# Performance work log

Hardware: AMD Instinct MI355X
Metric: run time of the kernel (lower is better)

The kernel has to match this reference:

```python
import jax, jax.numpy as jnp
import numpy as np

N_NODES, IN_DIM, HID, LAT, N_EDGES = 50000, 3000, 512, 30, 800000
NEG_SLOPE = 0.2


def setup_inputs() -> dict:
    key = jax.random.key(0)
    ks = jax.random.split(key, 6)
    x = jax.random.normal(ks[0], (N_NODES, IN_DIM), dtype=jnp.float32)
    edge_index = jax.random.randint(ks[1], (2, N_EDGES), 0, N_NODES, dtype=jnp.int64)
    # xavier-normal-ish scales
    W1 = jax.random.normal(ks[2], (IN_DIM, HID), dtype=jnp.float32) * 0.02
    W2 = jax.random.normal(ks[3], (HID, LAT), dtype=jnp.float32) * 0.06
    att_src = jax.random.normal(ks[4], (HID,), dtype=jnp.float32) * 0.1
    att_dst = jax.random.normal(ks[5], (HID,), dtype=jnp.float32) * 0.1
    return {"x": x, "edge_index": edge_index, "W1": W1, "W2": W2,
            "att_src": att_src, "att_dst": att_dst}


def _segment_softmax(e, seg, num_segments):
    # numerically stable softmax over variable-degree dst neighborhoods
    m = jax.ops.segment_max(e, seg, num_segments=num_segments)
    m = jnp.where(jnp.isfinite(m), m, 0.0)  # empty segments -> 0, harmless
    p = jnp.exp(e - m[seg])
    s = jax.ops.segment_sum(p, seg, num_segments=num_segments)
    return p / (s[seg] + 1e-16)


def reference(x, edge_index, W1, W2, att_src, att_dst):
    N = x.shape[0]
    src, dst = edge_index[0], edge_index[1]  # messages flow src(j) -> dst(i)

    # ---- conv1: full GAT layer (heads=1, no self-loops, no bias) ----
    h1 = x @ W1                                   # [N, 512]
    a_src = h1 @ att_src                          # [N]
    a_dst = h1 @ att_dst                          # [N]
    e = jax.nn.leaky_relu(a_src[src] + a_dst[dst], NEG_SLOPE)  # [E]
    alpha = _segment_softmax(e, dst, N)           # [E] (also tied attn for conv3)
    agg1 = jax.ops.segment_sum(h1[src] * alpha[:, None], dst, num_segments=N)
    x1 = jax.nn.elu(agg1)                         # [N, 512]

    # ---- conv2: attention=False -> plain linear projection ----
    x2 = x1 @ W2                                  # [N, 30] (latent embedding)

    # ---- conv3: tied weights (W2^T) + tied attention from conv1 ----
    h3 = x2 @ W2.T                                # [N, 512]
    agg3 = jax.ops.segment_sum(h3[src] * alpha[:, None], dst, num_segments=N)
    x3 = jax.nn.elu(agg3)

    # ---- conv4: attention=False, tied weights (W1^T) ----
    x4 = x3 @ W1.T                                # [N, in_channels]
    return (x2, x4)
```

## Files before the change

kernel.cpp:

```cpp
#include <hip/hip_runtime.h>

#define N_NODES 50000
#define IN_DIM  3000
#define HID     512
#define LAT     30
#define N_EDGES 800000
#define M_PAD   50048
#define K1_PAD  3008
#define N4_PAD  3072

typedef __bf16 bf16;
typedef unsigned int uint;
typedef __attribute__((ext_vector_type(4))) float f32x4;
typedef __attribute__((ext_vector_type(8))) bf16 bf16x8;

__device__ __forceinline__ float bf2f(bf16 b){ return (float)b; }

__device__ __forceinline__ void gl16(const void* g, void* l){
  __builtin_amdgcn_global_load_lds(
      (const __attribute__((address_space(1))) void*)g,
      (__attribute__((address_space(3))) void*)l, 16, 0, 0);
}

__device__ __forceinline__ int xcd_swz(int orig, int nwg){
  int q = nwg >> 3, r = nwg & 7;
  int xcd = orig & 7, lid = orig >> 3;
  return (xcd < r ? xcd*(q+1) : r*(q+1) + (xcd-r)*q) + lid;
}

__device__ __forceinline__ bf16x8 cvt8v(f32x4 a, f32x4 b){
  bf16x8 r;
  r[0]=(bf16)a[0]; r[1]=(bf16)a[1]; r[2]=(bf16)a[2]; r[3]=(bf16)a[3];
  r[4]=(bf16)b[0]; r[5]=(bf16)b[1]; r[6]=(bf16)b[2]; r[7]=(bf16)b[3];
  return r;
}

__global__ void k_w1t(const float* __restrict__ W1, bf16* __restrict__ W1T){
  int k = blockIdx.x*256 + threadIdx.x;
  int n = blockIdx.y;
  if (k >= K1_PAD) return;
  float v = (k < IN_DIM) ? W1[(long)k*HID + n] : 0.f;
  W1T[(long)n*K1_PAD + k] = (bf16)v;
}
__global__ void k_w1p(const float* __restrict__ W1, bf16* __restrict__ W1P){
  int k = blockIdx.x*256 + threadIdx.x;
  int n = blockIdx.y;
  if (k >= HID) return;
  float v = (n < IN_DIM) ? W1[(long)n*HID + k] : 0.f;
  W1P[(long)n*HID + k] = (bf16)v;
}
__global__ void k_w2t(const float* __restrict__ W2, bf16* __restrict__ W2T){
  int k = blockIdx.x*256 + threadIdx.x;
  int n = blockIdx.y;
  if (k >= HID) return;
  float v = (n < LAT) ? W2[(long)k*LAT + n] : 0.f;
  W2T[(long)n*HID + k] = (bf16)v;
}
__global__ void k_w2p(const float* __restrict__ W2, bf16* __restrict__ W2P){
  int t = blockIdx.x*256 + threadIdx.x;
  if (t >= HID*32) return;
  int n = t >> 5, k = t & 31;
  W2P[t] = (bf16)((k < LAT) ? W2[(long)n*LAT + k] : 0.f);
}

__global__ __launch_bounds__(256) void gemm_xw1(
    const float* __restrict__ X, const bf16* __restrict__ Bw, bf16* __restrict__ C)
{
  __shared__ float Af[2][128*32];
  __shared__ bf16  Bl[2][128*32];
  const int NBX = HID/128;
  const int tid  = threadIdx.x;
  const int lane = tid & 63;
  const int w    = tid >> 6;
  const int wm   = (w >> 1) * 64, wn = (w & 1) * 64;
  const int wgid = xcd_swz(blockIdx.x, gridDim.x);
  const int col0 = (wgid % NBX) * 128, row0 = (wgid / NBX) * 128;

  f32x4 acc[4][4];
  #pragma unroll
  for (int mi=0;mi<4;mi++)
    #pragma unroll
    for (int ni=0;ni<4;ni++)
      acc[mi][ni] = (f32x4){0.f,0.f,0.f,0.f};

  const int ar  = tid >> 3;
  const int apc = tid & 7;
  const int ac4 = (apc ^ (ar & 7)) * 4;
  int aoff[4];
  #pragma unroll
  for (int i=0;i<4;i++)
    aoff[i] = min(row0 + i*32 + ar, N_NODES-1) * IN_DIM;

  const int sr = tid >> 2;
  const int sc = (tid & 3) * 16;
  const char* gB = (const char*)(Bw + (long)(col0 + sr) * K1_PAD) + sc;
  const long bstep = (long)64 * K1_PAD * 2;

#define STAGE1(buf, ks) do{                                             \
    int kcl_ = min((ks)*32 + ac4, IN_DIM-4);                            \
    char* lA_ = (char*)&Af[buf][0] + tid*16;                            \
    _Pragma("unroll")                                                   \
    for (int i_=0;i_<4;i_++)                                            \
      gl16(X + aoff[i_] + kcl_, lA_ + i_*4096);                         \
    char* lB_ = (char*)&Bl[buf][0] + sr*64 + sc;                        \
    gl16(gB + (long)(ks)*64,         lB_);                              \
    gl16(gB + (long)(ks)*64 + bstep, lB_ + 64*64);                      \
  }while(0)

  STAGE1(0, 0);
  asm volatile("s_waitcnt vmcnt(0)" ::: "memory");
  __builtin_amdgcn_s_barrier();

  for (int ks = 0; ks < 94; ks++){
    const int cur = ks & 1;
    if (ks + 1 < 94) STAGE1(cur^1, ks+1);

    const float* Ac = &Af[cur][0];
    const bf16*  Bc = &Bl[cur][0];
    const int g2 = (lane >> 4) * 2;
    bf16x8 af[4], bfr[4];
    #pragma unroll
    for (int mi=0;mi<4;mi++){
      int row = wm + mi*16 + (lane & 15);
      int rx  = row & 7;
      f32x4 f0 = *(const f32x4*)&Ac[row*32 + ((g2    ) ^ rx)*4];
      f32x4 f1 = *(const f32x4*)&Ac[row*32 + ((g2 + 1) ^ rx)*4];
      af[mi] = cvt8v(f0, f1);
    }
    #pragma unroll
    for (int ni=0;ni<4;ni++)
      bfr[ni] = *(const bf16x8*)&Bc[(wn + ni*16 + (lane & 15))*32 + (lane>>4)*8];
    #pragma unroll
    for (int mi=0;mi<4;mi++)
      #pragma unroll
      for (int ni=0;ni<4;ni++)
        acc[mi][ni] = __builtin_amdgcn_mfma_f32_16x16x32_bf16(af[mi], bfr[ni], acc[mi][ni], 0, 0, 0);

    asm volatile("s_waitcnt vmcnt(0)" ::: "memory");
    __builtin_amdgcn_s_barrier();
  }
#undef STAGE1

  const int crb  = (lane >> 4) * 4;
  const int ccol = lane & 15;
  #pragma unroll
  for (int mi=0;mi<4;mi++){
    #pragma unroll
    for (int v=0;v<4;v++){
      int r = row0 + wm + mi*16 + crb + v;
      if (r >= N_NODES) continue;
      #pragma unroll
      for (int ni=0;ni<4;ni++){
        int cc = col0 + wn + ni*16 + ccol;
        C[(long)r*HID + cc] = (bf16)acc[mi][ni][v];
      }
    }
  }
}

template<bool C_F32, bool ELU>
__global__ __launch_bounds__(256) void gemm_glds(
    const bf16* __restrict__ A, const bf16* __restrict__ B, void* __restrict__ Cp,
    int lda, int ldb, int Ksteps, int Mvalid, int Nvalid, int ldc, int NBX)
{
  __shared__ bf16 Alds[2][128*32];
  __shared__ bf16 Blds[2][128*32];
  const int tid  = threadIdx.x;
  const int lane = tid & 63;
  const int w    = tid >> 6;
  const int wm   = (w >> 1) * 64, wn = (w & 1) * 64;
  const int wgid = xcd_swz(blockIdx.x, gridDim.x);
  const int col0 = (wgid % NBX) * 128, row0 = (wgid / NBX) * 128;

  f32x4 acc[4][4];
  #pragma unroll
  for (int mi=0;mi<4;mi++)
    #pragma unroll
    for (int ni=0;ni<4;ni++)
      acc[mi][ni] = (f32x4){0.f,0.f,0.f,0.f};

  const int sr = tid >> 2;
  const int sc = (tid & 3) * 16;

  const char* ga = (const char*)(A + (long)(row0 + sr) * lda) + sc;
  const char* gb = (const char*)(B + (long)(col0 + sr) * ldb) + sc;
  const long astep = (long)64 * lda * 2;
  const long bstep = (long)64 * ldb * 2;

#define STAGE2(buf, ks) do{                                             \
    const long ko_ = (long)(ks) * 64;                                   \
    char* la_ = (char*)&Alds[buf][0] + sr*64 + sc;                      \
    char* lb_ = (char*)&Blds[buf][0] + sr*64 + sc;                      \
    gl16(ga + ko_,         la_);                                        \
    gl16(ga + ko_ + astep, la_ + 64*64);                                \
    gl16(gb + ko_,         lb_);                                        \
    gl16(gb + ko_ + bstep, lb_ + 64*64);                                \
  }while(0)

  STAGE2(0, 0);
  asm volatile("s_waitcnt vmcnt(0)" ::: "memory");
  __builtin_amdgcn_s_barrier();

  for (int ks = 0; ks < Ksteps; ks++){
    const int cur = ks & 1;
    if (ks + 1 < Ksteps) STAGE2(cur^1, ks+1);

    const bf16* Ac = &Alds[cur][0];
    const bf16* Bc = &Blds[cur][0];
    bf16x8 af[4], bfr[4];
    #pragma unroll
    for (int mi=0;mi<4;mi++)
      af[mi] = *(const bf16x8*)&Ac[(wm + mi*16 + (lane & 15))*32 + (lane>>4)*8];
    #pragma unroll
    for (int ni=0;ni<4;ni++)
      bfr[ni] = *(const bf16x8*)&Bc[(wn + ni*16 + (lane & 15))*32 + (lane>>4)*8];
    #pragma unroll
    for (int mi=0;mi<4;mi++)
      #pragma unroll
      for (int ni=0;ni<4;ni++)
        acc[mi][ni] = __builtin_amdgcn_mfma_f32_16x16x32_bf16(af[mi], bfr[ni], acc[mi][ni], 0, 0, 0);

    asm volatile("s_waitcnt vmcnt(0)" ::: "memory");
    __builtin_amdgcn_s_barrier();
  }
#undef STAGE2

  const int crb  = (lane >> 4) * 4;
  const int ccol = lane & 15;
  #pragma unroll
  for (int mi=0;mi<4;mi++){
    #pragma unroll
    for (int v=0;v<4;v++){
      int r = row0 + wm + mi*16 + crb + v;
      if (r >= Mvalid) continue;
      #pragma unroll
      for (int ni=0;ni<4;ni++){
        int c = col0 + wn + ni*16 + ccol;
        if (c >= Nvalid) continue;
        float val = acc[mi][ni][v];
        if (ELU) val = (val > 0.f) ? val : expm1f(val);
        if (C_F32) ((float*)Cp)[(long)r*ldc + c] = val;
        else       ((bf16*)Cp)[(long)r*ldc + c] = (bf16)val;
      }
    }
  }
}

__global__ void k_attdots(const bf16* __restrict__ h1, const float* __restrict__ att_s,
                          const float* __restrict__ att_d, float* __restrict__ a_src,
                          float* __restrict__ a_dst){
  int gid = blockIdx.x * blockDim.x + threadIdx.x;
  int row = gid >> 6, lane = gid & 63;
  if (row >= N_NODES) return;
  bf16x8 hv = *(const bf16x8*)(h1 + (long)row*HID + lane*8);
  float s1 = 0.f, s2 = 0.f;
  #pragma unroll
  for (int j=0;j<8;j++){
    float h = bf2f(hv[j]);
    s1 = fmaf(h, att_s[lane*8+j], s1);
    s2 = fmaf(h, att_d[lane*8+j], s2);
  }
  #pragma unroll
  for (int o=32;o>0;o>>=1){ s1 += __shfl_down(s1,o); s2 += __shfl_down(s2,o); }
  if (lane == 0){ a_src[row] = s1; a_dst[row] = s2; }
}

__global__ void k_deg(const int* __restrict__ ei, int* __restrict__ deg){
  int e = blockIdx.x*256 + threadIdx.x;
  if (e >= N_EDGES) return;
  atomicAdd(&deg[ei[N_EDGES + e]], 1);
}

__global__ void k_scan(const int* __restrict__ deg, int* __restrict__ off, int* __restrict__ cur){
  const int n = M_PAD, T = 1024;
  int t = threadIdx.x;
  const int per = (n + T - 1) / T;
  int s0 = t*per, s1 = min(n, s0+per);
  int sum = 0;
  for (int i=s0;i<s1;i++) sum += deg[i];
  __shared__ int sd[1024];
  sd[t] = sum; __syncthreads();
  for (int o=1;o<T;o<<=1){
    int x = (t>=o) ? sd[t-o] : 0;
    __syncthreads();
    sd[t] += x;
    __syncthreads();
  }
  int run = sd[t] - sum;
  for (int i=s0;i<s1;i++){
    off[i] = run; cur[i] = run;
    run += deg[i];
  }
  if (s0 < n && s1 == n) off[n] = run;
}

__global__ void k_fill(const int* __restrict__ ei, int* __restrict__ cur,
                       int* __restrict__ csr_src, const float* __restrict__ a_s,
                       const float* __restrict__ a_d, float* __restrict__ p_e){
  int e = blockIdx.x*256 + threadIdx.x;
  if (e >= N_EDGES) return;
  int s = ei[e];
  int d = ei[N_EDGES + e];
  int pos = atomicAdd(&cur[d], 1);
  csr_src[pos] = s;
  float v = a_s[s] + a_d[d];
  v = (v > 0.f) ? v : 0.2f*v;
  p_e[pos] = __expf(v);
}

__global__ __launch_bounds__(512) void k_agg1(
    const int* __restrict__ off, const int* __restrict__ csr_src,
    const float* __restrict__ p_edge,
    const bf16* __restrict__ h1, bf16* __restrict__ x1,
    float* __restrict__ s_node)
{
  const int i = blockIdx.x;
  const int t = threadIdx.x;
  const int start = off[i];
  const int deg = off[i+1] - start;
  __shared__ float p_sh[512];
  __shared__ int   s_sh[512];

  float acc = 0.f, ssum = 0.f;
  for (int base=0; base<deg; base+=512){
    int cnt = min(512, deg-base);
    if (t < cnt){
      p_sh[t] = p_edge[start+base+t];
      s_sh[t] = csr_src[start+base+t];
    }
    __syncthreads();
    for (int k=0;k<cnt;k++){
      float pk = p_sh[k];
      ssum += pk;
      acc = fmaf(pk, bf2f(h1[(long)s_sh[k]*HID + t]), acc);
    }
    __syncthreads();
  }
  float val = acc / (ssum + 1e-16f);
  val = (val > 0.f) ? val : expm1f(val);
  x1[(long)i*HID + t] = (bf16)val;
  if (t == 0) s_node[i] = ssum;
}

__global__ void k_agg3(const int* __restrict__ off, const int* __restrict__ csr_src,
                       const float* __restrict__ p_edge, const float* __restrict__ s_node,
                       const float* __restrict__ x2, bf16* __restrict__ aggb)
{
  int i = blockIdx.x*8 + (threadIdx.x >> 5);
  int lane = threadIdx.x & 31;
  if (i >= M_PAD) return;
  float acc = 0.f;
  if (i < N_NODES){
    int s0 = off[i], d = off[i+1] - s0;
    for (int k=0;k<d;k++){
      int s = csr_src[s0+k];
      float pk = p_edge[s0+k];
      if (lane < LAT) acc = fmaf(pk, x2[(long)s*LAT + lane], acc);
    }
    acc *= 1.f/(s_node[i] + 1e-16f);
  }
  aggb[(long)i*32 + lane] = (bf16)((lane < LAT) ? acc : 0.f);
}

extern "C" void kernel_launch(void* const* d_in, const int* in_sizes, int n_in,
                              void* d_out, int out_size, void* d_ws, size_t ws_size,
                              hipStream_t stream)
{
  const float* x     = (const float*)d_in[0];
  const int*   ei    = (const int*)d_in[1];
  const float* W1    = (const float*)d_in[2];
  const float* W2    = (const float*)d_in[3];
  const float* att_s = (const float*)d_in[4];
  const float* att_d = (const float*)d_in[5];

  float* out_x2 = (float*)d_out;
  float* out_x4 = (float*)d_out + (long)N_NODES*LAT;

  bf16* h1 = (bf16*)out_x4;
  bf16* x1 = h1 + (long)M_PAD*HID;

  char* w = (char*)d_ws;
  bf16* W1T = (bf16*)w;  w += (long)HID*K1_PAD*2;
  bf16* W1P = (bf16*)w;  w += (long)N4_PAD*HID*2;
  bf16* W2T = (bf16*)w;  w += (long)128*HID*2;
  bf16* W2P = (bf16*)w;  w += (long)HID*32*2;
  bf16* x3  = (bf16*)w;  w += (long)M_PAD*HID*2;
  bf16* aggb= (bf16*)w;  w += (long)M_PAD*32*2;
  int* deg  = (int*)w;   w += (long)M_PAD*4;
  int* offs = (int*)w;   w += (long)(M_PAD+64)*4;
  int* cur  = (int*)w;   w += (long)M_PAD*4;
  int* csr  = (int*)w;   w += (long)N_EDGES*4;
  float* p_e = (float*)w; w += (long)N_EDGES*4;
  float* s_n = (float*)w; w += (long)M_PAD*4;
  float* a_s = (float*)w; w += (long)M_PAD*4;
  float* a_d = (float*)w; w += (long)M_PAD*4;

  k_w1t<<<dim3((K1_PAD+255)/256, HID), 256, 0, stream>>>(W1, W1T);
  k_w1p<<<dim3((HID+255)/256, N4_PAD), 256, 0, stream>>>(W1, W1P);
  k_w2t<<<dim3(2, 128), 256, 0, stream>>>(W2, W2T);
  k_w2p<<<(HID*32+255)/256, 256, 0, stream>>>(W2, W2P);

  hipMemsetAsync(deg, 0, (size_t)M_PAD*4, stream);
  k_deg<<<(N_EDGES+255)/256, 256, 0, stream>>>(ei, deg);
  k_scan<<<1, 1024, 0, stream>>>(deg, offs, cur);

  gemm_xw1<<<(M_PAD/128)*(HID/128), 256, 0, stream>>>(x, W1T, h1);

  k_attdots<<<(N_NODES*64)/256, 256, 0, stream>>>(h1, att_s, att_d, a_s, a_d);

  k_fill<<<(N_EDGES+255)/256, 256, 0, stream>>>(ei, cur, csr, a_s, a_d, p_e);

  k_agg1<<<N_NODES, 512, 0, stream>>>(offs, csr, p_e, h1, x1, s_n);

  gemm_glds<true,false><<<1*(M_PAD/128), 256, 0, stream>>>(
      x1, W2T, out_x2, HID, HID, HID/32, N_NODES, LAT, LAT, 1);

  k_agg3<<<(M_PAD+7)/8, 256, 0, stream>>>(offs, csr, p_e, s_n, out_x2, aggb);
  gemm_glds<false,true><<<(HID/128)*(M_PAD/128), 256, 0, stream>>>(
      aggb, W2P, x3, 32, 32, 1, M_PAD, HID, HID, HID/128);

  gemm_glds<true,false><<<(N4_PAD/128)*(M_PAD/128), 256, 0, stream>>>(
      x3, W1P, out_x4, HID, HID, HID/32, N_NODES, IN_DIM, IN_DIM, N4_PAD/128);
}
```

Before: 1.281 ms.

## Pipeline GEMM loads with partial waits, swizzle W1T, warp-per-node aggregation

```diff
diff --git a/kernel.cpp b/kernel.cpp
--- a/kernel.cpp
+++ b/kernel.cpp
@@ -40,7 +40,9 @@
   int n = blockIdx.y;
   if (k >= K1_PAD) return;
   float v = (k < IN_DIM) ? W1[(long)k*HID + n] : 0.f;
-  W1T[(long)n*K1_PAD + k] = (bf16)v;
+  int kt = k >> 5, c = (k >> 3) & 3, off = k & 7;
+  int p = (c + (n >> 1)) & 3;
+  W1T[(long)n*K1_PAD + kt*32 + p*8 + off] = (bf16)v;
 }
 __global__ void k_w1p(const float* __restrict__ W1, bf16* __restrict__ W1P){
   int k = blockIdx.x*256 + threadIdx.x;
@@ -63,7 +65,7 @@
   W2P[t] = (bf16)((k < LAT) ? W2[(long)n*LAT + k] : 0.f);
 }
 
-__global__ __launch_bounds__(256) void gemm_xw1(
+__global__ __launch_bounds__(256) void gemm_xf(
     const float* __restrict__ X, const bf16* __restrict__ Bw, bf16* __restrict__ C)
 {
   __shared__ float Af[2][128*32];
@@ -83,63 +85,69 @@
     for (int ni=0;ni<4;ni++)
       acc[mi][ni] = (f32x4){0.f,0.f,0.f,0.f};
 
-  const int ar  = tid >> 3;
-  const int apc = tid & 7;
-  const int ac4 = (apc ^ (ar & 7)) * 4;
-  int aoff[4];
-  #pragma unroll
-  for (int i=0;i<4;i++)
-    aoff[i] = min(row0 + i*32 + ar, N_NODES-1) * IN_DIM;
-
-  const int sr = tid >> 2;
-  const int sc = (tid & 3) * 16;
-  const char* gB = (const char*)(Bw + (long)(col0 + sr) * K1_PAD) + sc;
-  const long bstep = (long)64 * K1_PAD * 2;
-
-#define STAGE1(buf, ks) do{                                             \
-    int kcl_ = min((ks)*32 + ac4, IN_DIM-4);                            \
-    char* lA_ = (char*)&Af[buf][0] + tid*16;                            \
-    _Pragma("unroll")                                                   \
-    for (int i_=0;i_<4;i_++)                                            \
-      gl16(X + aoff[i_] + kcl_, lA_ + i_*4096);                         \
-    char* lB_ = (char*)&Bl[buf][0] + sr*64 + sc;                        \
-    gl16(gB + (long)(ks)*64,         lB_);                              \
-    gl16(gB + (long)(ks)*64 + bstep, lB_ + 64*64);                      \
+  const int s_arow = tid >> 3;
+  const int s_alog4 = ((tid & 7) ^ (s_arow & 7)) * 4;
+  long ar0 = (long)min(row0 +  0 + s_arow, N_NODES-1) * IN_DIM;
+  long ar1 = (long)min(row0 + 32 + s_arow, N_NODES-1) * IN_DIM;
+  long ar2 = (long)min(row0 + 64 + s_arow, N_NODES-1) * IN_DIM;
+  long ar3 = (long)min(row0 + 96 + s_arow, N_NODES-1) * IN_DIM;
+  const long boff0 = (long)(col0 +      (tid >> 2)) * K1_PAD + (tid & 3)*8;
+  const long boff1 = (long)(col0 + 64 + (tid >> 2)) * K1_PAD + (tid & 3)*8;
+
+#define STAGE_X(buf, ks) do{                                            \
+    const int kb_ = (ks)*32;                                            \
+    const int kc_ = min(kb_ + s_alog4, IN_DIM-4);                       \
+    char* la_ = (char*)&Af[buf][0] + tid*16;                            \
+    gl16(X + ar0 + kc_, la_);                                           \
+    gl16(X + ar1 + kc_, la_ + 4096);                                    \
+    gl16(X + ar2 + kc_, la_ + 8192);                                    \
+    gl16(X + ar3 + kc_, la_ + 12288);                                   \
+    char* lb_ = (char*)&Bl[buf][0] + tid*16;                            \
+    gl16(Bw + boff0 + kb_, lb_);                                        \
+    gl16(Bw + boff1 + kb_, lb_ + 4096);                                 \
   }while(0)
 
-  STAGE1(0, 0);
-  asm volatile("s_waitcnt vmcnt(0)" ::: "memory");
-  __builtin_amdgcn_s_barrier();
+  STAGE_X(0, 0);
+
+  const int g  = lane >> 4;
+  const int rl = lane & 15;
 
   for (int ks = 0; ks < 94; ks++){
     const int cur = ks & 1;
-    if (ks + 1 < 94) STAGE1(cur^1, ks+1);
+    if (ks + 1 < 94){
+      STAGE_X(cur^1, ks+1);
+      asm volatile("s_waitcnt vmcnt(6)" ::: "memory");
+    } else {
+      asm volatile("s_waitcnt vmcnt(0)" ::: "memory");
+    }
+    __builtin_amdgcn_s_barrier();
 
     const float* Ac = &Af[cur][0];
     const bf16*  Bc = &Bl[cur][0];
-    const int g2 = (lane >> 4) * 2;
     bf16x8 af[4], bfr[4];
     #pragma unroll
     for (int mi=0;mi<4;mi++){
-      int row = wm + mi*16 + (lane & 15);
-      int rx  = row & 7;
-      f32x4 f0 = *(const f32x4*)&Ac[row*32 + ((g2    ) ^ rx)*4];
-      f32x4 f1 = *(const f32x4*)&Ac[row*32 + ((g2 + 1) ^ rx)*4];
+      int r  = wm + mi*16 + rl;
+      int x7 = r & 7;
+      f32x4 f0 = *(const f32x4*)&Ac[r*32 + ((2*g    ) ^ x7)*4];
+      f32x4 f1 = *(const f32x4*)&Ac[r*32 + ((2*g + 1) ^ x7)*4];
       af[mi] = cvt8v(f0, f1);
     }
     #pragma unroll
-    for (int ni=0;ni<4;ni++)
-      bfr[ni] = *(const bf16x8*)&Bc[(wn + ni*16 + (lane & 15))*32 + (lane>>4)*8];
+    for (int ni=0;ni<4;ni++){
+      int r = wn + ni*16 + rl;
+      int p = (g + (r >> 1)) & 3;
+      bfr[ni] = *(const bf16x8*)((const char*)Bc + r*64 + p*16);
+    }
     #pragma unroll
     for (int mi=0;mi<4;mi++)
       #pragma unroll
       for (int ni=0;ni<4;ni++)
         acc[mi][ni] = __builtin_amdgcn_mfma_f32_16x16x32_bf16(af[mi], bfr[ni], acc[mi][ni], 0, 0, 0);
 
-    asm volatile("s_waitcnt vmcnt(0)" ::: "memory");
     __builtin_amdgcn_s_barrier();
   }
-#undef STAGE1
+#undef STAGE_X
 
   const int crb  = (lane >> 4) * 4;
   const int ccol = lane & 15;
@@ -181,13 +189,12 @@
 
   const int sr = tid >> 2;
   const int sc = (tid & 3) * 16;
-
   const char* ga = (const char*)(A + (long)(row0 + sr) * lda) + sc;
   const char* gb = (const char*)(B + (long)(col0 + sr) * ldb) + sc;
   const long astep = (long)64 * lda * 2;
   const long bstep = (long)64 * ldb * 2;
 
-#define STAGE2(buf, ks) do{                                             \
+#define STAGE_G(buf, ks) do{                                            \
     const long ko_ = (long)(ks) * 64;                                   \
     char* la_ = (char*)&Alds[buf][0] + sr*64 + sc;                      \
     char* lb_ = (char*)&Blds[buf][0] + sr*64 + sc;                      \
@@ -197,13 +204,17 @@
     gl16(gb + ko_ + bstep, lb_ + 64*64);                                \
   }while(0)
 
-  STAGE2(0, 0);
-  asm volatile("s_waitcnt vmcnt(0)" ::: "memory");
-  __builtin_amdgcn_s_barrier();
+  STAGE_G(0, 0);
 
   for (int ks = 0; ks < Ksteps; ks++){
     const int cur = ks & 1;
-    if (ks + 1 < Ksteps) STAGE2(cur^1, ks+1);
+    if (ks + 1 < Ksteps){
+      STAGE_G(cur^1, ks+1);
+      asm volatile("s_waitcnt vmcnt(4)" ::: "memory");
+    } else {
+      asm volatile("s_waitcnt vmcnt(0)" ::: "memory");
+    }
+    __builtin_amdgcn_s_barrier();
 
     const bf16* Ac = &Alds[cur][0];
     const bf16* Bc = &Blds[cur][0];
@@ -220,10 +231,9 @@
       for (int ni=0;ni<4;ni++)
         acc[mi][ni] = __builtin_amdgcn_mfma_f32_16x16x32_bf16(af[mi], bfr[ni], acc[mi][ni], 0, 0, 0);
 
-    asm volatile("s_waitcnt vmcnt(0)" ::: "memory");
     __builtin_amdgcn_s_barrier();
   }
-#undef STAGE2
+#undef STAGE_G
 
   const int crb  = (lane >> 4) * 4;
   const int ccol = lane & 15;
@@ -308,38 +318,41 @@
   p_e[pos] = __expf(v);
 }
 
-__global__ __launch_bounds__(512) void k_agg1(
+__global__ __launch_bounds__(256) void k_agg1w(
     const int* __restrict__ off, const int* __restrict__ csr_src,
     const float* __restrict__ p_edge,
     const bf16* __restrict__ h1, bf16* __restrict__ x1,
     float* __restrict__ s_node)
 {
-  const int i = blockIdx.x;
-  const int t = threadIdx.x;
+  const int i = blockIdx.x*4 + (threadIdx.x >> 6);
+  const int lane = threadIdx.x & 63;
+  if (i >= N_NODES) return;
   const int start = off[i];
   const int deg = off[i+1] - start;
-  __shared__ float p_sh[512];
-  __shared__ int   s_sh[512];
-
-  float acc = 0.f, ssum = 0.f;
-  for (int base=0; base<deg; base+=512){
-    int cnt = min(512, deg-base);
-    if (t < cnt){
-      p_sh[t] = p_edge[start+base+t];
-      s_sh[t] = csr_src[start+base+t];
-    }
-    __syncthreads();
-    for (int k=0;k<cnt;k++){
-      float pk = p_sh[k];
-      ssum += pk;
-      acc = fmaf(pk, bf2f(h1[(long)s_sh[k]*HID + t]), acc);
-    }
-    __syncthreads();
-  }
-  float val = acc / (ssum + 1e-16f);
-  val = (val > 0.f) ? val : expm1f(val);
-  x1[(long)i*HID + t] = (bf16)val;
-  if (t == 0) s_node[i] = ssum;
+
+  float acc[8];
+  #pragma unroll
+  for (int j=0;j<8;j++) acc[j] = 0.f;
+  float ssum = 0.f;
+
+  for (int k=0;k<deg;k++){
+    int s = csr_src[start+k];
+    float pk = p_edge[start+k];
+    ssum += pk;
+    bf16x8 hv = *(const bf16x8*)(h1 + (long)s*HID + lane*8);
+    #pragma unroll
+    for (int j=0;j<8;j++) acc[j] = fmaf(pk, bf2f(hv[j]), acc[j]);
+  }
+  float inv = 1.f/(ssum + 1e-16f);
+  bf16x8 o;
+  #pragma unroll
+  for (int j=0;j<8;j++){
+    float v = acc[j]*inv;
+    v = (v > 0.f) ? v : expm1f(v);
+    o[j] = (bf16)v;
+  }
+  *(bf16x8*)(x1 + (long)i*HID + lane*8) = o;
+  if (lane == 0) s_node[i] = ssum;
 }
 
 __global__ void k_agg3(const int* __restrict__ off, const int* __restrict__ csr_src,
@@ -404,13 +417,13 @@
   k_deg<<<(N_EDGES+255)/256, 256, 0, stream>>>(ei, deg);
   k_scan<<<1, 1024, 0, stream>>>(deg, offs, cur);
 
-  gemm_xw1<<<(M_PAD/128)*(HID/128), 256, 0, stream>>>(x, W1T, h1);
+  gemm_xf<<<(M_PAD/128)*(HID/128), 256, 0, stream>>>(x, W1T, h1);
 
   k_attdots<<<(N_NODES*64)/256, 256, 0, stream>>>(h1, att_s, att_d, a_s, a_d);
 
   k_fill<<<(N_EDGES+255)/256, 256, 0, stream>>>(ei, cur, csr, a_s, a_d, p_e);
 
-  k_agg1<<<N_NODES, 512, 0, stream>>>(offs, csr, p_e, h1, x1, s_n);
+  k_agg1w<<<(N_NODES+3)/4, 256, 0, stream>>>(offs, csr, p_e, h1, x1, s_n);
 
   gemm_glds<true,false><<<1*(M_PAD/128), 256, 0, stream>>>(
       x1, W2T, out_x2, HID, HID, HID/32, N_NODES, LAT, LAT, 1);
```

Result: faster. 1.161 ms (-9.4%).
